# Kernel tuning notes

Hardware: AMD Instinct MI355X
Metric: run time of the kernel (lower is better)

## Reference

```python
import jax, jax.numpy as jnp
import numpy as np

NUM_HEAD = 8
HEAD_DIM = 64
LMK = 32          # num_landmarks
WIN = 128         # window_size
DIM = 512         # transformer_dim == num_head*head_dim
EXT = WIN // 2    # ext_len in get_tiles_v2
TILE = 2 * EXT + WIN  # 256
SCALE = 1.0 / np.sqrt(HEAD_DIM)
NEG_INF = float('-inf')


def layernorm(x, g, b, eps=1e-5):
    m = jnp.mean(x, axis=-1, keepdims=True)
    v = jnp.mean((x - m) ** 2, axis=-1, keepdims=True)
    return (x - m) * jax.lax.rsqrt(v + eps) * g + b


def split_heads(x):
    b, s, _ = x.shape
    return x.reshape(b, s, NUM_HEAD, HEAD_DIM).transpose(0, 2, 1, 3)


def setup_inputs() -> dict:
    key = jax.random.key(0)
    ks = jax.random.split(key, 8)
    B, S = 2, 8192
    w = lambda k, sh: (jax.random.normal(k, sh, jnp.float32) * 0.02)
    return {
        'X': jax.random.normal(ks[0], (B, S, DIM), jnp.float32),
        'mask': jnp.ones((B, S), jnp.bool_),
        'Wq_w': w(ks[1], (DIM, DIM)), 'Wq_b': jnp.zeros((DIM,), jnp.float32),
        'Wk_w': w(ks[2], (DIM, DIM)), 'Wk_b': jnp.zeros((DIM,), jnp.float32),
        'Wv_w': w(ks[3], (DIM, DIM)), 'Wv_b': jnp.zeros((DIM,), jnp.float32),
        'Wo_w': w(ks[4], (DIM, DIM)), 'Wo_b': jnp.zeros((DIM,), jnp.float32),
        'ln_l_g': jnp.ones((DIM,), jnp.float32), 'ln_l_b': jnp.zeros((DIM,), jnp.float32),
        'ln_s_g': jnp.ones((DIM,), jnp.float32), 'ln_s_b': jnp.zeros((DIM,), jnp.float32),
        'dconv_w': w(ks[5], (DIM, NUM_HEAD * LMK)), 'dconv_b': jnp.zeros((NUM_HEAD * LMK,), jnp.float32),
    }


def reference(X, mask, Wq_w, Wq_b, Wk_w, Wk_b, Wv_w, Wv_b, Wo_w, Wo_b,
              ln_l_g, ln_l_b, ln_s_g, ln_s_b, dconv_w, dconv_b):
    B, S, D = X.shape
    G = S // WIN  # number of window groups
    pad_mask = ~mask  # True where padded

    Q = split_heads(X @ Wq_w + Wq_b) * SCALE                       # [B,H,S,dh]
    K = split_heads(layernorm(X @ Wk_w + Wk_b, ln_l_g, ln_l_b))    # [B,H,S,dh]
    V = split_heads(layernorm(X @ Wv_w + Wv_b, ln_l_g, ln_l_b))    # [B,H,S,dh]

    # --- landmark (long-range) compression ---
    hs = X @ dconv_w + dconv_b                                     # [B,S,H*L]
    hs = jnp.where(pad_mask[:, :, None], NEG_INF, hs)
    hs = jax.nn.softmax(hs.astype(jnp.float32), axis=1).astype(X.dtype)
    hs = hs.reshape(B, S, NUM_HEAD, LMK).transpose(0, 2, 3, 1)     # [B,H,L,S]
    K_c = jnp.einsum('bhls,bhsd->bhld', hs, K)                     # [B,H,L,dh]
    V_c = jnp.einsum('bhls,bhsd->bhld', hs, V)
    # dual LayerNorm on compressed keys/values (over combined head dim)
    K_c = split_heads(layernorm(K_c.transpose(0, 2, 1, 3).reshape(B, LMK, D), ln_s_g, ln_s_b))
    V_c = split_heads(layernorm(V_c.transpose(0, 2, 1, 3).reshape(B, LMK, D), ln_s_g, ln_s_b))

    attn_compress = jnp.einsum('bhsd,bhld->bhsl', Q, K_c)          # [B,H,S,L]

    # --- sliding-window (short-range) scores, v2 tiling ---
    idx = jnp.arange(G)[:, None] * WIN + jnp.arange(TILE)[None, :]  # [G,TILE] indices into padded seq
    K_pad = jnp.pad(K, ((0, 0), (0, 0), (EXT, EXT), (0, 0)))
    K_tiles = K_pad[:, :, idx, :]                                   # [B,H,G,TILE,dh]
    mask_pad = jnp.pad(pad_mask, ((0, 0), (EXT, EXT)), constant_values=True)
    mask_tiles = mask_pad[:, idx]                                   # [B,G,TILE]
    Q_tiles = Q.reshape(B, NUM_HEAD, G, WIN, HEAD_DIM)
    win = jnp.einsum('bhgwd,bhgtd->bhgwt', Q_tiles, K_tiles)
    win = jnp.where(mask_tiles[:, None, :, None, :], NEG_INF, win)
    win = win.reshape(B, NUM_HEAD, S, TILE)

    # --- joint softmax over [landmarks | window] ---
    all_scores = jnp.concatenate([attn_compress, win], axis=-1)     # [B,H,S,L+TILE]
    probs = jax.nn.softmax(all_scores.astype(jnp.float32), axis=-1).astype(X.dtype)
    probs = jnp.where(pad_mask[:, None, :, None], 0.0, probs)

    C = jnp.einsum('bhsl,bhld->bhsd', probs[..., :LMK], V_c)        # landmark contribution
    win_p = probs[..., LMK:].reshape(B, NUM_HEAD, G, WIN, TILE)
    V_pad = jnp.pad(V, ((0, 0), (0, 0), (EXT, EXT), (0, 0)))
    V_tiles = V_pad[:, :, idx, :]                                   # [B,H,G,TILE,dh]
    C = C + jnp.einsum('bhgwt,bhgtd->bhgwd', win_p, V_tiles).reshape(B, NUM_HEAD, S, HEAD_DIM)

    out = C.transpose(0, 2, 1, 3).reshape(B, S, D) @ Wo_w + Wo_b
    return out
```

## Files before the change

kernel.cpp:

```cpp
#include <hip/hip_runtime.h>

typedef unsigned short u16;
typedef unsigned int u32;
typedef __attribute__((ext_vector_type(8))) short bf16x8;
typedef __attribute__((ext_vector_type(4))) float f32x4;
typedef __attribute__((ext_vector_type(2))) float f32x2;

#define DEVI static __device__ __forceinline__

DEVI float bf2f(u16 u){ u32 x = ((u32)u) << 16; float f; __builtin_memcpy(&f, &x, 4); return f; }
DEVI u16 f2bf(float f){ u32 x; __builtin_memcpy(&x, &f, 4); u32 r = x + 0x7FFFu + ((x >> 16) & 1u); return (u16)(r >> 16); }
DEVI u32 pk2(float a, float b){ return ((u32)f2bf(b) << 16) | (u32)f2bf(a); }

DEVI f32x4 mfma16(bf16x8 a, bf16x8 b, f32x4 c){
  return __builtin_amdgcn_mfma_f32_16x16x32_bf16(a, b, c, 0, 0, 0);
}

typedef __attribute__((address_space(3))) u32* lds_ptr_t;
typedef const __attribute__((address_space(1))) u32* gbl_ptr_t;
DEVI void gload16(const void* g, const void* l){
  __builtin_amdgcn_global_load_lds((gbl_ptr_t)(unsigned long long)g,
                                   (lds_ptr_t)(unsigned long long)l,
                                   16, 0, 0);
}

__global__ void prep_kernel(const float* __restrict__ X, u16* __restrict__ Xb,
                            const float* __restrict__ Wq, const float* __restrict__ Wk,
                            const float* __restrict__ Wv, const float* __restrict__ Wd,
                            const float* __restrict__ Wo,
                            const float* __restrict__ Wqb, const float* __restrict__ Wkb,
                            const float* __restrict__ Wvb, const float* __restrict__ Wdb,
                            u16* __restrict__ WT, float* __restrict__ biasAll)
{
  __shared__ __align__(16) char pbuf[4224];
  if (blockIdx.x < 4096){
    int i = blockIdx.x * 256 + threadIdx.x;
    const f32x4* p = (const f32x4*)X;
    f32x4 a = p[(size_t)i*2], c = p[(size_t)i*2 + 1];
    bf16x8 v;
    v[0]=(short)f2bf(a[0]); v[1]=(short)f2bf(a[1]); v[2]=(short)f2bf(a[2]); v[3]=(short)f2bf(a[3]);
    v[4]=(short)f2bf(c[0]); v[5]=(short)f2bf(c[1]); v[6]=(short)f2bf(c[2]); v[7]=(short)f2bf(c[3]);
    *(bf16x8*)(Xb + (size_t)i*8) = v;
    return;
  }
  int id = blockIdx.x - 4096;
  if (id >= 1152){
    int c = (id - 1152) * 256 + threadIdx.x;
    float v = (c < 512) ? Wqb[c] : (c < 1024) ? Wkb[c-512] : (c < 1536) ? Wvb[c-1024] : Wdb[c-1536];
    biasAll[c] = v;
    return;
  }
  const float* W; int RO, N, local;
  if      (id < 256){ W = Wq; RO = 0;    N = 512; local = id; }
  else if (id < 512){ W = Wk; RO = 512;  N = 512; local = id - 256; }
  else if (id < 768){ W = Wv; RO = 1024; N = 512; local = id - 512; }
  else if (id < 896){ W = Wd; RO = 1536; N = 256; local = id - 768; }
  else              { W = Wo; RO = 1792; N = 512; local = id - 896; }
  int ntiles = N >> 5;
  int n0 = (local & (ntiles - 1)) * 32, k0 = (local / ntiles) * 32;
  float (*tile)[33] = (float(*)[33])pbuf;
  int tx = threadIdx.x & 31, ty = threadIdx.x >> 5;
  #pragma unroll
  for (int i = 0; i < 32; i += 8)
    tile[ty + i][tx] = W[(size_t)(k0 + ty + i) * N + n0 + tx];
  __syncthreads();
  #pragma unroll
  for (int i = 0; i < 32; i += 8)
    WT[(size_t)(RO + n0 + ty + i) * 512 + k0 + tx] = f2bf(tile[tx][ty + i]);
}

template<int MODE>
__global__ __launch_bounds__(256, 2) void gemmP(
    const u16* __restrict__ Abase, const u16* __restrict__ WT, const float* __restrict__ biasAll,
    u16* __restrict__ Qb, u16* __restrict__ Kb, u16* __restrict__ Vb,
    float* __restrict__ hsf, float* __restrict__ cmx, float* __restrict__ csm,
    float* __restrict__ pstatV, float* __restrict__ Cf)
{
  __shared__ __align__(16) u16 smem[32768];
  const int t = threadIdx.x, lane = t & 63, w = t >> 6;
  const int wm = w >> 1, wn = w & 1;
  const int lrow = lane & 15, lk = lane >> 4;
  const u16* Bbase = (MODE == 0) ? WT : (WT + (size_t)1792*512);
  const int srow = w*32 + (lane >> 3);
  const int scol = ((lane & 7) ^ (lane >> 3)) * 8;
  const int swz = (lrow & 7);
  const int NCH = (MODE == 0) ? 1792 : 512;
  const f32x4 fz = {0.f,0.f,0.f,0.f};

  for (int ch = blockIdx.x; ch < NCH; ch += 512){
    int by, bx;
    {
      int xcd = ch & 7, c = ch >> 3;
      if (MODE == 0){ by = xcd*16 + c/14;   bx = c % 14; }
      else          { by = xcd*16 + (c>>2); bx = c & 3; }
    }
    const int m0 = by*128, n0 = bx*128;
    const u16* sA = Abase + (size_t)(m0 + srow)*512 + scol;
    const u16* sB = Bbase + (size_t)(n0 + srow)*512 + scol;

    f32x4 acc[4][4];
    #pragma unroll
    for (int i = 0; i < 4; i++)
      #pragma unroll
      for (int j = 0; j < 4; j++) acc[i][j] = fz;

    auto stage = [&](int tt){
      int slot = tt & 1;
      #pragma unroll
      for (int i = 0; i < 4; i++){
        gload16(sA + tt*64 + (size_t)i*4096, smem + slot*8192 + (w*4 + i)*512);
        gload16(sB + tt*64 + (size_t)i*4096, smem + 16384 + slot*8192 + (w*4 + i)*512);
      }
    };

    stage(0);
    stage(1);

    #pragma unroll
    for (int tt = 0; tt < 8; tt++){
      if (tt < 7) asm volatile("s_waitcnt vmcnt(8)" ::: "memory");
      else        asm volatile("s_waitcnt vmcnt(0)" ::: "memory");
      __builtin_amdgcn_s_barrier();
      const u16* aS = smem + (tt & 1)*8192;
      const u16* bS = smem + 16384 + (tt & 1)*8192;
      #pragma unroll
      for (int ks = 0; ks < 2; ks++){
        bf16x8 af[4], bfv[4];
        #pragma unroll
        for (int mi = 0; mi < 4; mi++){
          int r = wm*64 + mi*16 + lrow;
          af[mi] = *(const bf16x8*)(aS + (r*8 + ((ks*4 + lk) ^ swz))*8);
        }
        #pragma unroll
        for (int ni = 0; ni < 4; ni++){
          int r = wn*64 + ni*16 + lrow;
          bfv[ni] = *(const bf16x8*)(bS + (r*8 + ((ks*4 + lk) ^ swz))*8);
        }
        #pragma unroll
        for (int mi = 0; mi < 4; mi++)
          #pragma unroll
          for (int ni = 0; ni < 4; ni++)
            acc[mi][ni] = mfma16(bfv[ni], af[mi], acc[mi][ni]);
      }
      __builtin_amdgcn_s_barrier();
      if (tt + 2 < 8) stage(tt + 2);
    }

    if (MODE == 1){
      #pragma unroll
      for (int mi = 0; mi < 4; mi++){
        int grow = m0 + wm*64 + mi*16 + lrow;
        #pragma unroll
        for (int ni = 0; ni < 4; ni++){
          int gcol0 = n0 + wn*64 + ni*16 + lk*4;
          f32x4 bv4 = *(const f32x4*)(biasAll + gcol0);
          f32x4 vv;
          #pragma unroll
          for (int rr = 0; rr < 4; rr++) vv[rr] = acc[mi][ni][rr] + bv4[rr];
          *(f32x4*)(Cf + (size_t)grow*512 + gcol0) = vv;
        }
      }
      continue;
    }

    if (bx < 12){
      const int sel = bx >> 2;
      u16* dst = (sel == 0) ? Qb : (sel == 1) ? Kb : Vb;
      const float scale = (sel == 0) ? 0.125f : 1.0f;
      f32x4 bv4s[4];
      #pragma unroll
      for (int ni = 0; ni < 4; ni++)
        bv4s[ni] = *(const f32x4*)(biasAll + n0 + wn*64 + ni*16 + lk*4);
      #pragma unroll
      for (int mi = 0; mi < 4; mi++){
        int grow = m0 + wm*64 + mi*16 + lrow;
        int b = grow >> 13, s = grow & 8191;
        #pragma unroll
        for (int ni = 0; ni < 4; ni++){
          int gcol0 = n0 + wn*64 + ni*16 + lk*4;
          int lcol0 = gcol0 & 511, hh = lcol0 >> 6, dd0 = lcol0 & 63;
          float v0 = (acc[mi][ni][0] + bv4s[ni][0]) * scale;
          float v1 = (acc[mi][ni][1] + bv4s[ni][1]) * scale;
          float v2 = (acc[mi][ni][2] + bv4s[ni][2]) * scale;
          float v3 = (acc[mi][ni][3] + bv4s[ni][3]) * scale;
          u32* p = (u32*)(dst + (((size_t)(b*8 + hh))*8192 + s)*64 + dd0);
          p[0] = pk2(v0, v1);
          p[1] = pk2(v2, v3);
        }
      }
      if (sel == 2){
        float* vst = (float*)smem;
        __syncthreads();
        #pragma unroll
        for (int mi = 0; mi < 4; mi++){
          float s = 0.f, q = 0.f;
          #pragma unroll
          for (int ni = 0; ni < 4; ni++)
            #pragma unroll
            for (int rr = 0; rr < 4; rr++){
              float v = acc[mi][ni][rr] + bv4s[ni][rr];
              s += v; q += v*v;
            }
          s += __shfl_xor(s, 16); q += __shfl_xor(q, 16);
          s += __shfl_xor(s, 32); q += __shfl_xor(q, 32);
          if (lk == 0){
            int rloc = wm*64 + mi*16 + lrow;
            vst[rloc*4 + wn*2]     = s;
            vst[rloc*4 + wn*2 + 1] = q;
          }
        }
        __syncthreads();
        if (t < 128){
          float s = vst[t*4+0] + vst[t*4+2];
          float q = vst[t*4+1] + vst[t*4+3];
          pstatV[(size_t)(m0 + t)*8 + (bx - 8)*2]     = s;
          pstatV[(size_t)(m0 + t)*8 + (bx - 8)*2 + 1] = q;
        }
      }
    } else {
      float* pm = (float*)smem;
      float* ps = pm + 256;
      __syncthreads();
      #pragma unroll
      for (int ni = 0; ni < 4; ni++){
        int gcol0 = n0 + wn*64 + ni*16 + lk*4;
        int c0 = gcol0 - 1536;
        f32x4 bv4 = *(const f32x4*)(biasAll + gcol0);
        float mx[4], sm[4];
        #pragma unroll
        for (int rr = 0; rr < 4; rr++){ mx[rr] = -1e30f; sm[rr] = 0.f; }
        #pragma unroll
        for (int mi = 0; mi < 4; mi++){
          int grow = m0 + wm*64 + mi*16 + lrow;
          f32x4 v;
          #pragma unroll
          for (int rr = 0; rr < 4; rr++){
            v[rr] = acc[mi][ni][rr] + bv4[rr];
            float nm = fmaxf(mx[rr], v[rr]);
            sm[rr] = sm[rr]*__expf(mx[rr] - nm) + __expf(v[rr] - nm);
            mx[rr] = nm;
          }
          *(f32x4*)(hsf + (size_t)grow*256 + c0) = v;
        }
        #pragma unroll
        for (int rr = 0; rr < 4; rr++){
          #pragma unroll
          for (int d2 = 1; d2 < 16; d2 <<= 1){
            float om = __shfl_xor(mx[rr], d2), os = __shfl_xor(sm[rr], d2);
            float nm = fmaxf(mx[rr], om);
            sm[rr] = sm[rr]*__expf(mx[rr] - nm) + os*__expf(om - nm);
            mx[rr] = nm;
          }
        }
        if (lrow == 0){
          int cl = wn*64 + ni*16 + lk*4;
          f32x4 m4 = {mx[0], mx[1], mx[2], mx[3]};
          f32x4 s4 = {sm[0], sm[1], sm[2], sm[3]};
          *(f32x4*)(pm + wm*128 + cl) = m4;
          *(f32x4*)(ps + wm*128 + cl) = s4;
        }
      }
      __syncthreads();
      if (t < 128){
        float ma = pm[t], mb = pm[128 + t];
        float nm = fmaxf(ma, mb);
        float s = ps[t]*__expf(ma - nm) + ps[128 + t]*__expf(mb - nm);
        int b = m0 >> 13, chunk = (m0 & 8191) >> 7;
        int c = (n0 - 1536) + t;
        cmx[((size_t)b*64 + chunk)*256 + c] = nm;
        csm[((size_t)b*64 + chunk)*256 + c] = s;
      }
    }
    __syncthreads();
  }
}

__global__ __launch_bounds__(256) void mid_kernel(
    const u16* __restrict__ Kb, float* __restrict__ kstat,
    const u16* __restrict__ Vb, const float* __restrict__ pstatV,
    const float* __restrict__ gg, const float* __restrict__ bb, u16* __restrict__ VbT,
    const float* __restrict__ cmax, const float* __restrict__ csum,
    float* __restrict__ gmax, float* __restrict__ gsum)
{
  __shared__ __align__(16) char mbuf[9216];
  const int bid = blockIdx.x;
  if (bid < 4096){
    const int lane = threadIdx.x & 63, w = threadIdx.x >> 6;
    const int row = bid * 4 + w;
    const int b = row >> 13, si = row & 8191;
    const int hh = lane >> 3, d = (lane & 7) * 8;
    const u16* p = Kb + (((size_t)(b*8 + hh))*8192 + si)*64 + d;
    bf16x8 raw = *(const bf16x8*)p;
    float x[8];
    #pragma unroll
    for (int j = 0; j < 8; j++) x[j] = bf2f((u16)raw[j]);
    float s = 0.f, q = 0.f;
    #pragma unroll
    for (int j = 0; j < 8; j++){ s += x[j]; q += x[j]*x[j]; }
    #pragma unroll
    for (int d2 = 1; d2 < 64; d2 <<= 1){ s += __shfl_xor(s, d2); q += __shfl_xor(q, d2); }
    float mean = s * (1.f/512.f);
    float var  = q * (1.f/512.f) - mean*mean;
    float rstd = rsqrtf(var + 1e-5f);
    if (lane == 0){
      kstat[(size_t)row*2]     = mean;
      kstat[(size_t)row*2 + 1] = rstd;
    }
    return;
  }
  if (bid < 6144){
    int id2 = bid - 4096;
    const int st = id2 & 127, bh = id2 >> 7;
    const int b = bh >> 3, h = bh & 7;
    const int t = threadIdx.x;
    u16 (*tile)[72] = (u16(*)[72])mbuf;
    {
      int row = t >> 2, cc = (t & 3) * 16;
      int grow = b*8192 + st*64 + row;
      f32x4 p0 = *(const f32x4*)(pstatV + (size_t)grow*8);
      f32x4 p1 = *(const f32x4*)(pstatV + (size_t)grow*8 + 4);
      float mean = (p0[0]+p0[2]+p1[0]+p1[2]) * (1.f/512.f);
      float msq  = (p0[1]+p0[3]+p1[1]+p1[3]) * (1.f/512.f);
      float rstd = rsqrtf(msq - mean*mean + 1e-5f);
      const u16* src = Vb + ((size_t)bh*8192 + st*64 + row)*64 + cc;
      bf16x8 v0 = *(const bf16x8*)src, v1 = *(const bf16x8*)(src + 8);
      #pragma unroll
      for (int j = 0; j < 8; j++){
        int c = h*64 + cc + j;
        tile[row][cc + j]     = f2bf((bf2f((u16)v0[j]) - mean)*rstd*gg[c] + bb[c]);
        int c2 = c + 8;
        tile[row][cc + 8 + j] = f2bf((bf2f((u16)v1[j]) - mean)*rstd*gg[c2] + bb[c2]);
      }
    }
    __syncthreads();
    {
      int d = t >> 2, sc4 = (t & 3) * 16;
      bf16x8 o0, o1;
      #pragma unroll
      for (int i = 0; i < 8; i++) o0[i] = (short)tile[sc4 + i][d];
      #pragma unroll
      for (int i = 0; i < 8; i++) o1[i] = (short)tile[sc4 + 8 + i][d];
      u16* dst = VbT + ((size_t)bh*64 + d)*8192 + st*64 + sc4;
      *(bf16x8*)dst       = o0;
      *(bf16x8*)(dst + 8) = o1;
    }
    return;
  }
  {
    int b = bid - 6144, c = threadIdx.x;
    float m[4], s[4];
    #pragma unroll
    for (int u = 0; u < 4; u++){ m[u] = -1e30f; s[u] = 0.f; }
    for (int ch = 0; ch < 64; ch += 4){
      #pragma unroll
      for (int u = 0; u < 4; u++){
        float cm = cmax[((size_t)b*64 + ch + u)*256 + c];
        float cs = csum[((size_t)b*64 + ch + u)*256 + c];
        float nm = fmaxf(m[u], cm);
        s[u] = s[u]*__expf(m[u] - nm) + cs*__expf(cm - nm);
        m[u] = nm;
      }
    }
    #pragma unroll
    for (int u = 1; u < 4; u++){
      float nm = fmaxf(m[0], m[u]);
      s[0] = s[0]*__expf(m[0]-nm) + s[u]*__expf(m[u]-nm);
      m[0] = nm;
    }
    gmax[b*256 + c] = m[0]; gsum[b*256 + c] = s[0];
  }
}

__global__ __launch_bounds__(256) void cmp2_kernel(const float* __restrict__ hsf,
    const float* __restrict__ gmax, const float* __restrict__ gsum,
    const u16* __restrict__ Kb, const u16* __restrict__ Vb,
    const float* __restrict__ kstat, const float* __restrict__ pstatV,
    const float* __restrict__ gg, const float* __restrict__ bb,
    float* __restrict__ pK, float* __restrict__ pV)
{
  __shared__ __align__(16) u16 Pt[32*72];
  __shared__ __align__(16) u16 Kt[64*72];
  __shared__ __align__(16) u16 Vt[64*72];
  const int sch = blockIdx.x, bh = blockIdx.y;
  const int b = bh >> 3, h = bh & 7;
  const int t = threadIdx.x, lane = t & 63, w = t >> 6;
  const int lrow = lane & 15, lk = lane >> 4;
  const int sl = lane;
  float gm[8], gi[8];
  #pragma unroll
  for (int j = 0; j < 8; j++){
    int c = h*32 + w*8 + j;
    gm[j] = gmax[b*256 + c];
    gi[j] = 1.0f / gsum[b*256 + c];
  }
  float glv[16], blv[16];
  #pragma unroll
  for (int j = 0; j < 16; j++){
    int c = h*64 + w*16 + j;
    glv[j] = gg[c]; blv[j] = bb[c];
  }
  const f32x4 fz = {0.f,0.f,0.f,0.f};
  f32x4 aK[2], aV[2];
  aK[0]=fz; aK[1]=fz; aV[0]=fz; aV[1]=fz;

  for (int tile = 0; tile < 4; ++tile){
    int s0 = sch*256 + tile*64;
    int grow = b*8192 + s0 + sl;
    {
      const float* src = hsf + (size_t)grow*256 + h*32 + w*8;
      f32x4 x0 = *(const f32x4*)src, x1 = *(const f32x4*)(src + 4);
      #pragma unroll
      for (int j = 0; j < 4; j++){
        Pt[(w*8 + j)*72 + sl]     = f2bf(__expf(x0[j] - gm[j])   * gi[j]);
        Pt[(w*8 + 4 + j)*72 + sl] = f2bf(__expf(x1[j] - gm[4+j]) * gi[4+j]);
      }
    }
    {
      f32x2 st = *(const f32x2*)(kstat + (size_t)grow*2);
      const u16* ks = Kb + ((size_t)bh*8192 + s0 + sl)*64 + w*16;
      bf16x8 k0 = *(const bf16x8*)ks, k1 = *(const bf16x8*)(ks + 8);
      #pragma unroll
      for (int j = 0; j < 8; j++){
        Kt[(w*16 + j)*72 + sl]     = f2bf((bf2f((u16)k0[j]) - st[0])*st[1]*glv[j]   + blv[j]);
        Kt[(w*16 + 8 + j)*72 + sl] = f2bf((bf2f((u16)k1[j]) - st[0])*st[1]*glv[8+j] + blv[8+j]);
      }
    }
    {
      f32x4 p0 = *(const f32x4*)(pstatV + (size_t)grow*8);
      f32x4 p1 = *(const f32x4*)(pstatV + (size_t)grow*8 + 4);
      float mean = (p0[0]+p0[2]+p1[0]+p1[2]) * (1.f/512.f);
      float msq  = (p0[1]+p0[3]+p1[1]+p1[3]) * (1.f/512.f);
      float rstd = rsqrtf(msq - mean*mean + 1e-5f);
      const u16* vs = Vb + ((size_t)bh*8192 + s0 + sl)*64 + w*16;
      bf16x8 v0 = *(const bf16x8*)vs, v1 = *(const bf16x8*)(vs + 8);
      #pragma unroll
      for (int j = 0; j < 8; j++){
        Vt[(w*16 + j)*72 + sl]     = f2bf((bf2f((u16)v0[j]) - mean)*rstd*glv[j]   + blv[j]);
        Vt[(w*16 + 8 + j)*72 + sl] = f2bf((bf2f((u16)v1[j]) - mean)*rstd*glv[8+j] + blv[8+j]);
      }
    }
    __syncthreads();
    #pragma unroll
    for (int ks = 0; ks < 2; ks++){
      bf16x8 a0 = *(const bf16x8*)(Pt + (lrow)*72      + ks*32 + lk*8);
      bf16x8 a1 = *(const bf16x8*)(Pt + (16 + lrow)*72 + ks*32 + lk*8);
      bf16x8 bK = *(const bf16x8*)(Kt + (w*16 + lrow)*72 + ks*32 + lk*8);
      bf16x8 bV = *(const bf16x8*)(Vt + (w*16 + lrow)*72 + ks*32 + lk*8);
      aK[0] = mfma16(a0, bK, aK[0]);
      aK[1] = mfma16(a1, bK, aK[1]);
      aV[0] = mfma16(a0, bV, aV[0]);
      aV[1] = mfma16(a1, bV, aV[1]);
    }
    __syncthreads();
  }
  size_t base = ((size_t)bh*32 + sch)*2048;
  #pragma unroll
  for (int li = 0; li < 2; li++){
    #pragma unroll
    for (int r = 0; r < 4; r++){
      size_t o = base + (size_t)(li*16 + lk*4 + r)*64 + w*16 + lrow;
      pK[o] = aK[li][r];
      pV[o] = aV[li][r];
    }
  }
}

__global__ __launch_bounds__(256) void ln_c_kernel(const float* __restrict__ pK, const float* __restrict__ pV,
    const float* __restrict__ gg, const float* __restrict__ bb,
    u16* __restrict__ Kcb, u16* __restrict__ VcT)
{
  __shared__ float red[4][4];
  const int b = blockIdx.x >> 5, l = blockIdx.x & 31;
  const int t = threadIdx.x, lane = t & 63, w = t >> 6;
  float xk[2], xv[2];
  #pragma unroll
  for (int q2 = 0; q2 < 2; q2++){
    int c = t + q2*256;
    int hh = c >> 6, d = c & 63;
    float sk = 0.f, sv = 0.f;
    for (int ch = 0; ch < 32; ch++){
      size_t idx = (((size_t)(b*8 + hh)*32 + ch)*2048) + l*64 + d;
      sk += pK[idx]; sv += pV[idx];
    }
    xk[q2] = sk; xv[q2] = sv;
  }
  float s1 = xk[0]+xk[1], q1 = xk[0]*xk[0]+xk[1]*xk[1];
  float s2 = xv[0]+xv[1], q2s = xv[0]*xv[0]+xv[1]*xv[1];
  #pragma unroll
  for (int d2 = 1; d2 < 64; d2 <<= 1){
    s1 += __shfl_xor(s1, d2); q1 += __shfl_xor(q1, d2);
    s2 += __shfl_xor(s2, d2); q2s += __shfl_xor(q2s, d2);
  }
  if (lane == 0){ red[0][w]=s1; red[1][w]=q1; red[2][w]=s2; red[3][w]=q2s; }
  __syncthreads();
  s1 = red[0][0]+red[0][1]+red[0][2]+red[0][3];
  q1 = red[1][0]+red[1][1]+red[1][2]+red[1][3];
  s2 = red[2][0]+red[2][1]+red[2][2]+red[2][3];
  q2s = red[3][0]+red[3][1]+red[3][2]+red[3][3];
  float mk = s1*(1.f/512.f), vk = q1*(1.f/512.f) - mk*mk, rk = rsqrtf(vk + 1e-5f);
  float mv = s2*(1.f/512.f), vvv = q2s*(1.f/512.f) - mv*mv, rv = rsqrtf(vvv + 1e-5f);
  #pragma unroll
  for (int q2 = 0; q2 < 2; q2++){
    int c = t + q2*256;
    int hh = c >> 6, d = c & 63;
    Kcb[(((size_t)(b*8 + hh))*32 + l)*64 + d] = f2bf((xk[q2]-mk)*rk*gg[c] + bb[c]);
    VcT[(((size_t)(b*8 + hh))*64 + d)*32 + l] = f2bf((xv[q2]-mv)*rv*gg[c] + bb[c]);
  }
}

__global__ __launch_bounds__(512, 4) void attn2_kernel(
    const u16* __restrict__ Qb, const u16* __restrict__ Kb, const u16* __restrict__ Kcb,
    const u16* __restrict__ VbT, const u16* __restrict__ VcT,
    const float* __restrict__ kstat, const float* __restrict__ lnlg, const float* __restrict__ lnlb,
    u16* __restrict__ Cb)
{
  __shared__ __align__(16) char smem[74752];
  u16* Vt = (u16*)(smem + 36864);
  u16* Pl = (u16*)smem;

  const int g = (blockIdx.x & 7) * 8 + (blockIdx.x >> 3);
  const int h = blockIdx.y, b = blockIdx.z;
  const int bh = b*8 + h;
  const int t = threadIdx.x, lane = t & 63, w = t >> 6;
  const int lrow = lane & 15, lk = lane >> 4;
  const int s0 = g*128 - 64;
  const bf16x8 bz = {0,0,0,0,0,0,0,0};
  const f32x4 fz = {0.f,0.f,0.f,0.f};

  float g8[8], b8[8];
  {
    int kcl = t & 7;
    #pragma unroll
    for (int j = 0; j < 8; j++){
      int c = h*64 + kcl*8 + j;
      g8[j] = lnlg[c]; b8[j] = lnlb[c];
    }
  }

  #pragma unroll
  for (int it = 0; it < 5; it++){
    int idx = it*512 + t;
    if (idx < 2304){
      int row = idx >> 3, kc = idx & 7;
      bf16x8 v = bz;
      if (row < 256){
        int sk = s0 + row;
        if (sk >= 0 && sk < 8192){
          v = *(const bf16x8*)(Kb + ((size_t)bh*8192 + sk)*64 + kc*8);
          f32x2 st = *(const f32x2*)(kstat + (size_t)(b*8192 + sk)*2);
          #pragma unroll
          for (int j = 0; j < 8; j++)
            v[j] = (short)f2bf((bf2f((u16)v[j]) - st[0])*st[1]*g8[j] + b8[j]);
        }
      } else {
        v = *(const bf16x8*)(Kcb + ((size_t)bh*32 + (row - 256))*64 + kc*8);
      }
      int off = row*128 + kc*16; off ^= (row & 7) << 4;
      *(bf16x8*)(smem + off) = v;
    }
  }
  #pragma unroll
  for (int it = 0; it < 4; it++){
    int idx = it*512 + t;
    int d = idx >> 5, cc = idx & 31;
    int sk = s0 + cc*8;
    bf16x8 v = bz;
    if (sk >= 0 && sk < 8192) v = *(const bf16x8*)(VbT + ((size_t)bh*64 + d)*8192 + sk);
    *(bf16x8*)(Vt + d*296 + cc*8) = v;
  }
  if (t < 256){
    int d = t >> 2, cc = t & 3;
    bf16x8 v = *(const bf16x8*)(VcT + ((size_t)bh*64 + d)*32 + cc*8);
    *(bf16x8*)(Vt + d*296 + 256 + cc*8) = v;
  }
  bf16x8 qf[2];
  #pragma unroll
  for (int ks = 0; ks < 2; ks++)
    qf[ks] = *(const bf16x8*)(Qb + ((size_t)bh*8192 + g*128 + w*16 + lrow)*64 + ks*32 + lk*8);

  __syncthreads();

  f32x4 sc[18];
  #pragma unroll
  for (int j = 0; j < 18; j++) sc[j] = fz;
  __builtin_amdgcn_s_setprio(1);
  #pragma unroll
  for (int j = 0; j < 18; j++){
    int row = j*16 + lrow;
    #pragma unroll
    for (int ks = 0; ks < 2; ks++){
      int off = row*128 + ks*64 + lk*16; off ^= (row & 7) << 4;
      bf16x8 kf = *(const bf16x8*)(smem + off);
      sc[j] = mfma16(kf, qf[ks], sc[j]);
    }
  }
  __builtin_amdgcn_s_setprio(0);

  #pragma unroll
  for (int j = 0; j < 16; j++){
    int sb = s0 + j*16 + lk*4;
    if (sb < 0 || sb >= 8192){
      sc[j][0] = -1e30f; sc[j][1] = -1e30f; sc[j][2] = -1e30f; sc[j][3] = -1e30f;
    }
  }

  float m = -1e30f;
  #pragma unroll
  for (int j = 0; j < 18; j++)
    m = fmaxf(m, fmaxf(fmaxf(sc[j][0], sc[j][1]), fmaxf(sc[j][2], sc[j][3])));
  m = fmaxf(m, __shfl_xor(m, 16));
  m = fmaxf(m, __shfl_xor(m, 32));
  float ssum = 0.f;
  #pragma unroll
  for (int j = 0; j < 18; j++){
    #pragma unroll
    for (int r = 0; r < 4; r++){
      float e = __expf(sc[j][r] - m);
      sc[j][r] = e; ssum += e;
    }
  }
  ssum += __shfl_xor(ssum, 16);
  ssum += __shfl_xor(ssum, 32);
  float inv = 1.0f / ssum;

  f32x4 ao[4];
  #pragma unroll
  for (int nj = 0; nj < 4; nj++) ao[nj] = fz;
  const int prow = w*16 + lrow;

  #pragma unroll
  for (int c = 0; c < 3; c++){
    __syncthreads();
    #pragma unroll
    for (int jj = 0; jj < 6; jj++){
      int j = c*6 + jj;
      u32* dst = (u32*)(Pl + prow*104 + jj*16 + lk*4);
      dst[0] = pk2(sc[j][0], sc[j][1]);
      dst[1] = pk2(sc[j][2], sc[j][3]);
    }
    __syncthreads();
    __builtin_amdgcn_s_setprio(1);
    #pragma unroll
    for (int ksl = 0; ksl < 3; ksl++){
      bf16x8 pb = *(const bf16x8*)(Pl + prow*104 + ksl*32 + lk*8);
      #pragma unroll
      for (int nj = 0; nj < 4; nj++){
        bf16x8 av = *(const bf16x8*)(Vt + (nj*16 + lrow)*296 + c*96 + ksl*32 + lk*8);
        ao[nj] = mfma16(av, pb, ao[nj]);
      }
    }
    __builtin_amdgcn_s_setprio(0);
  }

  const int qglob = g*128 + w*16 + lrow;
  #pragma unroll
  for (int nj = 0; nj < 4; nj++){
    u32* dst = (u32*)(Cb + ((size_t)b*8192 + qglob)*512 + h*64 + nj*16 + lk*4);
    dst[0] = pk2(ao[nj][0]*inv, ao[nj][1]*inv);
    dst[1] = pk2(ao[nj][2]*inv, ao[nj][3]*inv);
  }
}

constexpr size_t OFF_XB   = 0;
constexpr size_t OFF_WT   = OFF_XB  + 16777216;
constexpr size_t OFF_QB   = OFF_WT  + 2359296;
constexpr size_t OFF_KB   = OFF_QB  + 16777216;
constexpr size_t OFF_VB   = OFF_KB  + 16777216;
constexpr size_t OFF_CB   = OFF_VB  + 16777216;
constexpr size_t OFF_VBT  = OFF_CB  + 16777216;
constexpr size_t OFF_HSF  = OFF_VBT + 16777216;
constexpr size_t OFF_CMX  = OFF_HSF + 16777216;
constexpr size_t OFF_CSM  = OFF_CMX + 131072;
constexpr size_t OFF_GMX  = OFF_CSM + 131072;
constexpr size_t OFF_GSM  = OFF_GMX + 2048;
constexpr size_t OFF_PK   = OFF_GSM + 2048;
constexpr size_t OFF_PV   = OFF_PK  + 4194304;
constexpr size_t OFF_KCB  = OFF_PV  + 4194304;
constexpr size_t OFF_VCT  = OFF_KCB + 65536;
constexpr size_t OFF_BIAS = OFF_VCT + 65536;
constexpr size_t OFF_PSV  = OFF_BIAS + 8192;
constexpr size_t OFF_KST  = OFF_PSV + 524288;

extern "C" void kernel_launch(void* const* d_in, const int* in_sizes, int n_in,
                              void* d_out, int out_size, void* d_ws, size_t ws_size,
                              hipStream_t stream)
{
  const float* X    = (const float*)d_in[0];
  const float* Wq   = (const float*)d_in[2];
  const float* Wqb  = (const float*)d_in[3];
  const float* Wk   = (const float*)d_in[4];
  const float* Wkb  = (const float*)d_in[5];
  const float* Wv   = (const float*)d_in[6];
  const float* Wvb  = (const float*)d_in[7];
  const float* Wo   = (const float*)d_in[8];
  const float* Wob  = (const float*)d_in[9];
  const float* lnlg = (const float*)d_in[10];
  const float* lnlb = (const float*)d_in[11];
  const float* lnsg = (const float*)d_in[12];
  const float* lnsb = (const float*)d_in[13];
  const float* Wd   = (const float*)d_in[14];
  const float* Wdb  = (const float*)d_in[15];
  float* out = (float*)d_out;

  char* ws = (char*)d_ws;
  u16*   Xb   = (u16*)(ws + OFF_XB);
  u16*   WT   = (u16*)(ws + OFF_WT);
  u16*   Qb   = (u16*)(ws + OFF_QB);
  u16*   Kb   = (u16*)(ws + OFF_KB);
  u16*   Vb   = (u16*)(ws + OFF_VB);
  u16*   Cbp  = (u16*)(ws + OFF_CB);
  u16*   VbT  = (u16*)(ws + OFF_VBT);
  float* hsf  = (float*)(ws + OFF_HSF);
  float* cmx  = (float*)(ws + OFF_CMX);
  float* csm  = (float*)(ws + OFF_CSM);
  float* gmx  = (float*)(ws + OFF_GMX);
  float* gsm  = (float*)(ws + OFF_GSM);
  float* pK   = (float*)(ws + OFF_PK);
  float* pV   = (float*)(ws + OFF_PV);
  u16*   Kcb  = (u16*)(ws + OFF_KCB);
  u16*   VcT  = (u16*)(ws + OFF_VCT);
  float* biasAll = (float*)(ws + OFF_BIAS);
  float* pstatV  = (float*)(ws + OFF_PSV);
  float* kstat   = (float*)(ws + OFF_KST);

  prep_kernel<<<dim3(5255), dim3(256), 0, stream>>>(X, Xb, Wq, Wk, Wv, Wd, Wo,
                                                    Wqb, Wkb, Wvb, Wdb, WT, biasAll);

  gemmP<0><<<dim3(512), dim3(256), 0, stream>>>(Xb, WT, biasAll, Qb, Kb, Vb,
                                                hsf, cmx, csm, pstatV, nullptr);

  mid_kernel<<<dim3(6146), dim3(256), 0, stream>>>(Kb, kstat, Vb, pstatV, lnlg, lnlb, VbT,
                                                   cmx, csm, gmx, gsm);

  cmp2_kernel<<<dim3(32,16), dim3(256), 0, stream>>>(hsf, gmx, gsm, Kb, Vb, kstat, pstatV,
                                                     lnlg, lnlb, pK, pV);
  ln_c_kernel<<<dim3(64), dim3(256), 0, stream>>>(pK, pV, lnsg, lnsb, Kcb, VcT);

  attn2_kernel<<<dim3(64,8,2), dim3(512), 0, stream>>>(Qb, Kb, Kcb, VbT, VcT,
                                                       kstat, lnlg, lnlb, Cbp);

  gemmP<1><<<dim3(512), dim3(256), 0, stream>>>(Cbp, WT, Wob, nullptr, nullptr, nullptr,
                                                nullptr, nullptr, nullptr, nullptr, out);
}
```

Measured before the change: 164.2 us.

## Load GEMM B operand directly into registers instead of staging through LDS

In the projection GEMM, each wave now loads its B-operand (weight) fragments straight from global memory into double-buffered registers with inline-asm dwordx4 loads. Only the A tile still goes through LDS via global_load_lds, so LDS use is halved and the B-side LDS reads and swizzle work go away. The wait counts are retuned to the new number of in-flight loads. In exchange, B data is fetched separately by the two waves that share it, which doubles global/L2 traffic for weights. It also raises register pressure and relies on manual vmcnt accounting for asm loads the compiler does not track.

```diff
diff --git a/kernel.cpp b/kernel.cpp
--- a/kernel.cpp
+++ b/kernel.cpp
@@ -23,6 +23,14 @@
                                    (lds_ptr_t)(unsigned long long)l,
                                    16, 0, 0);
 }
+
+#define LOADB(PB, TT) do { \
+  _Pragma("unroll") \
+  for (int f_ = 0; f_ < 8; f_++){ \
+    asm volatile("global_load_dwordx4 %0, %1, off offset:%2" \
+                 : "=&v"(breg[PB][f_]) : "v"(bR[f_ & 3]), "i"((TT)*128 + (f_ >> 2)*64)); \
+  } \
+} while(0)
 
 __global__ void prep_kernel(const float* __restrict__ X, u16* __restrict__ Xb,
                             const float* __restrict__ Wq, const float* __restrict__ Wk,
@@ -76,7 +84,7 @@
     float* __restrict__ hsf, float* __restrict__ cmx, float* __restrict__ csm,
     float* __restrict__ pstatV, float* __restrict__ Cf)
 {
-  __shared__ __align__(16) u16 smem[32768];
+  __shared__ __align__(16) u16 smem[16384];
   const int t = threadIdx.x, lane = t & 63, w = t >> 6;
   const int wm = w >> 1, wn = w & 1;
   const int lrow = lane & 15, lk = lane >> 4;
@@ -96,7 +104,10 @@
     }
     const int m0 = by*128, n0 = bx*128;
     const u16* sA = Abase + (size_t)(m0 + srow)*512 + scol;
-    const u16* sB = Bbase + (size_t)(n0 + srow)*512 + scol;
+    const u16* bR[4];
+    #pragma unroll
+    for (int ni = 0; ni < 4; ni++)
+      bR[ni] = Bbase + (size_t)(n0 + wn*64 + ni*16 + lrow)*512 + lk*8;
 
     f32x4 acc[4][4];
     #pragma unroll
@@ -104,46 +115,49 @@
       #pragma unroll
       for (int j = 0; j < 4; j++) acc[i][j] = fz;
 
-    auto stage = [&](int tt){
+    bf16x8 breg[2][8];
+
+    auto stageA = [&](int tt){
       int slot = tt & 1;
       #pragma unroll
-      for (int i = 0; i < 4; i++){
+      for (int i = 0; i < 4; i++)
         gload16(sA + tt*64 + (size_t)i*4096, smem + slot*8192 + (w*4 + i)*512);
-        gload16(sB + tt*64 + (size_t)i*4096, smem + 16384 + slot*8192 + (w*4 + i)*512);
-      }
     };
 
-    stage(0);
-    stage(1);
+    LOADB(0, 0);
+    stageA(0);
+    stageA(1);
 
     #pragma unroll
     for (int tt = 0; tt < 8; tt++){
-      if (tt < 7) asm volatile("s_waitcnt vmcnt(8)" ::: "memory");
+      if (tt < 7) asm volatile("s_waitcnt vmcnt(4)" ::: "memory");
       else        asm volatile("s_waitcnt vmcnt(0)" ::: "memory");
       __builtin_amdgcn_s_barrier();
+      __builtin_amdgcn_sched_barrier(0);
+      if (tt == 0) LOADB(1, 1);
+      else if (tt == 1) LOADB(0, 2);
+      else if (tt == 2) LOADB(1, 3);
+      else if (tt == 3) LOADB(0, 4);
+      else if (tt == 4) LOADB(1, 5);
+      else if (tt == 5) LOADB(0, 6);
+      else if (tt == 6) LOADB(1, 7);
       const u16* aS = smem + (tt & 1)*8192;
-      const u16* bS = smem + 16384 + (tt & 1)*8192;
       #pragma unroll
       for (int ks = 0; ks < 2; ks++){
-        bf16x8 af[4], bfv[4];
+        bf16x8 af[4];
         #pragma unroll
         for (int mi = 0; mi < 4; mi++){
           int r = wm*64 + mi*16 + lrow;
           af[mi] = *(const bf16x8*)(aS + (r*8 + ((ks*4 + lk) ^ swz))*8);
         }
         #pragma unroll
-        for (int ni = 0; ni < 4; ni++){
-          int r = wn*64 + ni*16 + lrow;
-          bfv[ni] = *(const bf16x8*)(bS + (r*8 + ((ks*4 + lk) ^ swz))*8);
-        }
-        #pragma unroll
         for (int mi = 0; mi < 4; mi++)
           #pragma unroll
           for (int ni = 0; ni < 4; ni++)
-            acc[mi][ni] = mfma16(bfv[ni], af[mi], acc[mi][ni]);
+            acc[mi][ni] = mfma16(breg[tt & 1][ks*4 + ni], af[mi], acc[mi][ni]);
       }
       __builtin_amdgcn_s_barrier();
-      if (tt + 2 < 8) stage(tt + 2);
+      if (tt + 2 < 8) stageA(tt + 2);
     }
 
     if (MODE == 1){
```

Result: slower. 195.8 us (+19.2%).
